# Optimization experiments

Hardware: AMD Instinct MI355X
Metric: run time of the kernel (lower is better)

Reference implementation:

```python
import jax, jax.numpy as jnp
import numpy as np

EPS_SINKHORN = 0.01   # entropic regularization (cost / eps)
EPS_LOG = 1e-8        # numerical epsilon inside logs
NUM_ITERS = 50


def setup_inputs() -> dict:
    key = jax.random.key(0)
    k1, k2 = jax.random.split(key)
    B, N = 8, 2048
    x1 = jax.random.normal(k1, (B, N, 3), dtype=jnp.float32)
    x2 = jax.random.normal(k2, (B, N, 3), dtype=jnp.float32)
    return {"x1": x1, "x2": x2}


def reference(x1, x2):
    # x1, x2: [B, N, 3] point clouds
    B, N, _ = x1.shape
    # pairwise squared-distance cost matrix: [B, N, N]
    cost = jnp.sum((x1[:, :, None, :] - x2[:, None, :, :]) ** 2, axis=-1)
    K = jnp.exp(-cost / EPS_SINKHORN)  # constant across iterations

    inv_n = jnp.float32(1.0 / N)
    mu = jnp.full((B, N), inv_n, dtype=cost.dtype)
    nu = jnp.full((B, N), inv_n, dtype=cost.dtype)
    log_mu = jnp.log(mu + EPS_LOG)
    log_nu = jnp.log(nu + EPS_LOG)

    def step(carry, _):
        u, v = carry
        # row update: sum_j K_ij * exp(v_j)
        u = log_mu - jnp.log(jnp.einsum('bij,bj->bi', K, jnp.exp(v)) + EPS_LOG)
        # col update: sum_i K_ij * exp(u_i)
        v = log_nu - jnp.log(jnp.einsum('bij,bi->bj', K, jnp.exp(u)) + EPS_LOG)
        return (u, v), None

    u0 = jnp.zeros((B, N), dtype=cost.dtype)
    v0 = jnp.zeros((B, N), dtype=cost.dtype)
    (u, v), _ = jax.lax.scan(step, (u0, v0), None, length=NUM_ITERS)

    transport = K * jnp.exp(u[:, :, None] + v[:, None, :])  # [B, N, N]
    emd = jnp.sum(transport * cost, axis=(1, 2))            # [B]
    return emd
```

## Files before the change

kernel.cpp:

```cpp
#include <hip/hip_runtime.h>
#include <cmath>

#define BATCH 8
#define NPT   2048
#define NPAIR (NPT / 2)
#define NPTS  (BATCH * NPT)
#define TILES 64
#define GRID_MAIN 256
#define THREADS 1024
#define ITERS 50

#define C_LOG2E 1.4426950408889634f
#define NEG100C (-144.26950408889634f)
#define S200C   288.53900817779268f
#define EPS_LOG 1e-8f
#define LN2_01  0.006931471805599453f

typedef float v2f __attribute__((ext_vector_type(2)));
typedef float v4f __attribute__((ext_vector_type(4)));
typedef unsigned long long u64t;

static __device__ __forceinline__ float fast_exp2(float x) {
#if __has_builtin(__builtin_amdgcn_exp2f)
    return __builtin_amdgcn_exp2f(x);
#else
    return exp2f(x);
#endif
}

static __device__ __forceinline__ v2f pk_fma(v2f a, v2f b, v2f c) {
    v2f d;
    asm("v_pk_fma_f32 %0, %1, %2, %3" : "=v"(d) : "v"(a), "v"(b), "v"(c));
    return d;
}
static __device__ __forceinline__ v2f pk_add(v2f a, v2f b) {
    v2f d;
    asm("v_pk_add_f32 %0, %1, %2" : "=v"(d) : "v"(a), "v"(b));
    return d;
}

static __device__ __forceinline__ float gload(const float* p) {
    return __hip_atomic_load(p, __ATOMIC_RELAXED, __HIP_MEMORY_SCOPE_AGENT);
}
static __device__ __forceinline__ void gstore(float* p, float val) {
    __hip_atomic_store(p, val, __ATOMIC_RELAXED, __HIP_MEMORY_SCOPE_AGENT);
}
static __device__ __forceinline__ u64t gload2(const float* p) {
    return __hip_atomic_load((const u64t*)p, __ATOMIC_RELAXED,
                             __HIP_MEMORY_SCOPE_AGENT);
}

__global__ void init_kernel(float* __restrict__ out,
                            unsigned int* __restrict__ flags) {
    int t = threadIdx.x;
    if (t < BATCH) out[t] = 0.0f;
    flags[t] = 0u;
}

static __device__ __forceinline__ void bar_arrive(unsigned int* flags,
                                                  int slot, unsigned int ph) {
    __syncthreads();
    if (threadIdx.x == 0)
        __hip_atomic_store(&flags[slot], ph, __ATOMIC_RELAXED,
                           __HIP_MEMORY_SCOPE_AGENT);
}
static __device__ __forceinline__ void bar_wait(const unsigned int* bflags,
                                                int wave, int lane,
                                                unsigned int ph) {
    if (wave == 0) {
        while (__hip_atomic_load(&bflags[lane], __ATOMIC_RELAXED,
                                 __HIP_MEMORY_SCOPE_AGENT) < ph) {
            __builtin_amdgcn_s_sleep(1);
        }
    }
    __syncthreads();
    __builtin_amdgcn_sched_barrier(0);
}

static __device__ __forceinline__ float half_core(
        const v4f* cdXY, const v4f* cdZW, int p0,
        v2f RX, v2f RY, v2f RZ, v2f RC)
{
    float accx = 0.0f, accy = 0.0f;
#pragma unroll 4
    for (int s = 0; s < 32; s++) {
        v4f a  = cdXY[p0 + s];
        v4f bz = cdZW[p0 + s];
        v2f xx = __builtin_shufflevector(a,  a,  0, 1);
        v2f yy = __builtin_shufflevector(a,  a,  2, 3);
        v2f zz = __builtin_shufflevector(bz, bz, 0, 1);
        v2f ww = __builtin_shufflevector(bz, bz, 2, 3);
        v2f t = pk_fma(xx, RX, ww);
        t = pk_fma(yy, RY, t);
        t = pk_fma(zz, RZ, t);
        t = pk_add(t, RC);
        accx += fast_exp2(t.x);
        accy += fast_exp2(t.y);
    }
    return accx + accy;
}

__global__ __launch_bounds__(THREADS, 4) void sinkhorn_kernel(
        const float* __restrict__ x1, const float* __restrict__ x2,
        float* __restrict__ u, float* __restrict__ v,
        unsigned int* __restrict__ flags, float* __restrict__ out)
{
    __shared__ v4f c1XY[2][NPAIR], c1ZW[2][NPAIR];
    __shared__ v4f c2XY[2][NPAIR], c2ZW[2][NPAIR];
    __shared__ float part[32][17];

    const int b0   = blockIdx.x / TILES;
    const int tile = blockIdx.x % TILES;
    const int bA = b0, bB = b0 + 4;
    const int baseA = bA * NPT, baseB = bB * NPT;
    const int slotA = bA * TILES + tile, slotB = bB * TILES + tile;
    const unsigned int* flA = flags + bA * TILES;
    const unsigned int* flB = flags + bB * TILES;

    const int tid  = threadIdx.x;
    const int wave = tid >> 6;
    const int lane = tid & 63;
    const int rloc = lane & 31;
    const int ch   = lane >> 5;
    const int row  = tile * 32 + rloc;
    const int p0   = wave * 64 + ch * 32;

    const float log_mu = logf(1.0f / (float)NPT + EPS_LOG);

    float P1a[2], P1b[2], P2a[2], P2b[2];
#pragma unroll
    for (int g = 0; g < 2; g++) {
        int base = g ? baseB : baseA;
        const float* p = x1 + 3 * (base + 2 * tid);
        float ax = p[0], ay = p[1], az = p[2];
        float bx = p[3], by = p[4], bz = p[5];
        float na = fmaf(ax, ax, fmaf(ay, ay, az * az));
        float nb = fmaf(bx, bx, fmaf(by, by, bz * bz));
        P1a[g] = na * NEG100C;  P1b[g] = nb * NEG100C;
        c1XY[g][tid] = (v4f){ax * S200C, bx * S200C, ay * S200C, by * S200C};
        c1ZW[g][tid] = (v4f){az * S200C, bz * S200C, P1a[g], P1b[g]};

        p = x2 + 3 * (base + 2 * tid);
        ax = p[0]; ay = p[1]; az = p[2];
        bx = p[3]; by = p[4]; bz = p[5];
        na = fmaf(ax, ax, fmaf(ay, ay, az * az));
        nb = fmaf(bx, bx, fmaf(by, by, bz * bz));
        P2a[g] = na * NEG100C;  P2b[g] = nb * NEG100C;
        c2XY[g][tid] = (v4f){ax * S200C, bx * S200C, ay * S200C, by * S200C};
        c2ZW[g][tid] = (v4f){az * S200C, bz * S200C, P2a[g], P2b[g]};
    }

    v2f RX1[2], RY1[2], RZ1[2], RC1[2], RX2[2], RY2[2], RZ2[2], RC2[2];
    float rc1s[2];
#pragma unroll
    for (int g = 0; g < 2; g++) {
        int base = g ? baseB : baseA;
        const float* p = x1 + 3 * (base + row);
        float a = p[0], bb = p[1], c = p[2];
        float nn = NEG100C * fmaf(a, a, fmaf(bb, bb, c * c));
        RX1[g] = (v2f){a, a};  RY1[g] = (v2f){bb, bb};
        RZ1[g] = (v2f){c, c};  RC1[g] = (v2f){nn, nn};
        rc1s[g] = nn;
        p = x2 + 3 * (base + row);
        a = p[0]; bb = p[1]; c = p[2];
        nn = NEG100C * fmaf(a, a, fmaf(bb, bb, c * c));
        RX2[g] = (v2f){a, a};  RY2[g] = (v2f){bb, bb};
        RZ2[g] = (v2f){c, c};  RC2[g] = (v2f){nn, nn};
    }
    __syncthreads();

    auto reduce_store = [&](float s, float* dst) {
        s += __shfl_xor(s, 32, 64);
        if (lane < 32) part[rloc][wave] = s;
        __syncthreads();
        if (wave == 0) {
            float t = 0.0f;
#pragma unroll
            for (int w = 0; w < 16; w++) t += part[rloc][w];
            float res = log_mu - __logf(t + EPS_LOG);
            if (lane < 32) gstore(dst, res);
        }
    };
    auto fold_u = [&](int g) {
        u64t d = gload2(u + (g ? baseB : baseA) + 2 * tid);
        reinterpret_cast<v2f*>(&c1ZW[g][tid])[1] = (v2f){
            fmaf(C_LOG2E, __uint_as_float((unsigned)d), P1a[g]),
            fmaf(C_LOG2E, __uint_as_float((unsigned)(d >> 32)), P1b[g])};
        __syncthreads();
    };
    auto fold_v = [&](int g) {
        u64t d = gload2(v + (g ? baseB : baseA) + 2 * tid);
        reinterpret_cast<v2f*>(&c2ZW[g][tid])[1] = (v2f){
            fmaf(C_LOG2E, __uint_as_float((unsigned)d), P2a[g]),
            fmaf(C_LOG2E, __uint_as_float((unsigned)(d >> 32)), P2b[g])};
        __syncthreads();
    };
    auto comp_u = [&](int g) {
        float s = half_core(c2XY[g], c2ZW[g], p0,
                            RX1[g], RY1[g], RZ1[g], RC1[g]);
        reduce_store(s, u + (g ? baseB : baseA) + row);
    };
    auto comp_v = [&](int g) {
        float s = half_core(c1XY[g], c1ZW[g], p0,
                            RX2[g], RY2[g], RZ2[g], RC2[g]);
        reduce_store(s, v + (g ? baseB : baseA) + row);
    };

    comp_u(0); bar_arrive(flags, slotA, 1);
    comp_u(1); bar_arrive(flags, slotB, 1);

    for (int it = 0; it < ITERS; it++) {
        const unsigned pu = 2 * it + 1, pv = 2 * it + 2;
        bar_wait(flA, wave, lane, pu);
        fold_u(0);
        comp_v(0); bar_arrive(flags, slotA, pv);
        bar_wait(flB, wave, lane, pu);
        fold_u(1);
        comp_v(1); bar_arrive(flags, slotB, pv);
        bar_wait(flA, wave, lane, pv);
        fold_v(0);
        if (it < ITERS - 1) { comp_u(0); bar_arrive(flags, slotA, pu + 2); }
        bar_wait(flB, wave, lane, pv);
        fold_v(1);
        if (it < ITERS - 1) { comp_u(1); bar_arrive(flags, slotB, pu + 2); }
    }

    v2f* cvp0 = reinterpret_cast<v2f*>(c1XY[0]);
    v2f* cvp1 = reinterpret_cast<v2f*>(c1XY[1]);
    {
        u64t dA = gload2(v + baseA + 2 * tid);
        u64t dB = gload2(v + baseB + 2 * tid);
        cvp0[tid] = (v2f){0.01f * __uint_as_float((unsigned)dA),
                          0.01f * __uint_as_float((unsigned)(dA >> 32))};
        cvp1[tid] = (v2f){0.01f * __uint_as_float((unsigned)dB),
                          0.01f * __uint_as_float((unsigned)(dB >> 32))};
    }
    __syncthreads();

    const v2f NL2 = {-LN2_01, -LN2_01};
    float es[2];
#pragma unroll
    for (int g = 0; g < 2; g++) {
        int base = g ? baseB : baseA;
        v2f* cvp = g ? cvp1 : cvp0;
        float ur = gload(&u[base + row]);
        float rcs = fmaf(C_LOG2E, ur, rc1s[g]);
        v2f RCC = (v2f){rcs, rcs};
        float sus = 0.01f * ur;
        v2f SU = (v2f){sus, sus};
        v2f eacc = {0.0f, 0.0f};
#pragma unroll 4
        for (int s = 0; s < 32; s++) {
            v4f a   = c2XY[g][p0 + s];
            v4f bz  = c2ZW[g][p0 + s];
            v2f cv2 = cvp[p0 + s];
            v2f xx = __builtin_shufflevector(a,  a,  0, 1);
            v2f yy = __builtin_shufflevector(a,  a,  2, 3);
            v2f zz = __builtin_shufflevector(bz, bz, 0, 1);
            v2f ww = __builtin_shufflevector(bz, bz, 2, 3);
            v2f t = pk_fma(xx, RX1[g], ww);
            t = pk_fma(yy, RY1[g], t);
            t = pk_fma(zz, RZ1[g], t);
            t = pk_add(t, RCC);
            v2f c2 = pk_fma(t, NL2, pk_add(SU, cv2));
            eacc.x = fmaf(fast_exp2(t.x), c2.x, eacc.x);
            eacc.y = fmaf(fast_exp2(t.y), c2.y, eacc.y);
        }
        float e = eacc.x + eacc.y;
#pragma unroll
        for (int m = 32; m >= 1; m >>= 1) e += __shfl_xor(e, m, 64);
        es[g] = e;
    }

    if (lane == 0) { part[0][wave] = es[0]; part[1][wave] = es[1]; }
    __syncthreads();
    if (tid == 0) {
        float sA = 0.0f, sB = 0.0f;
#pragma unroll
        for (int w = 0; w < 16; w++) { sA += part[0][w]; sB += part[1][w]; }
        atomicAdd(&out[bA], sA);
        atomicAdd(&out[bB], sB);
    }
}

extern "C" void kernel_launch(void* const* d_in, const int* in_sizes, int n_in,
                              void* d_out, int out_size, void* d_ws, size_t ws_size,
                              hipStream_t stream) {
    (void)in_sizes; (void)n_in; (void)out_size; (void)ws_size;
    const float* x1 = (const float*)d_in[0];
    const float* x2 = (const float*)d_in[1];
    float* out = (float*)d_out;

    char* ws = (char*)d_ws;
    float* u = (float*)ws;
    float* v = u + NPTS;
    unsigned int* flags = (unsigned int*)(v + NPTS);

    init_kernel<<<1, 512, 0, stream>>>(out, flags);
    sinkhorn_kernel<<<GRID_MAIN, THREADS, 0, stream>>>(x1, x2, u, v, flags, out);
}
```

Measured before the change: 825.3 us.

## Register-block two rows per thread and drop per-fold block barriers

Each thread now handles two rows (16 lanes per row group instead of 32), so every shared-memory load of column data feeds two rows' distance and exp computations, halving LDS traffic per exp. The __syncthreads after fold_u/fold_v is removed and the final reduction reads partial sums as vec4 from a padded 16-byte-aligned buffer. The packed inline asm is replaced by plain vector arithmetic the compiler can schedule. Removing the fold barriers relies on the reduce barrier and bar_wait's __syncthreads for ordering, and the extra per-row registers raise register pressure.

```diff
diff --git a/kernel.cpp b/kernel.cpp
--- a/kernel.cpp
+++ b/kernel.cpp
@@ -28,17 +28,6 @@
 #endif
 }
 
-static __device__ __forceinline__ v2f pk_fma(v2f a, v2f b, v2f c) {
-    v2f d;
-    asm("v_pk_fma_f32 %0, %1, %2, %3" : "=v"(d) : "v"(a), "v"(b), "v"(c));
-    return d;
-}
-static __device__ __forceinline__ v2f pk_add(v2f a, v2f b) {
-    v2f d;
-    asm("v_pk_add_f32 %0, %1, %2" : "=v"(d) : "v"(a), "v"(b));
-    return d;
-}
-
 static __device__ __forceinline__ float gload(const float* p) {
     return __hip_atomic_load(p, __ATOMIC_RELAXED, __HIP_MEMORY_SCOPE_AGENT);
 }
@@ -64,11 +53,11 @@
         __hip_atomic_store(&flags[slot], ph, __ATOMIC_RELAXED,
                            __HIP_MEMORY_SCOPE_AGENT);
 }
-static __device__ __forceinline__ void bar_wait(const unsigned int* bflags,
+static __device__ __forceinline__ void bar_wait(const unsigned int* bf,
                                                 int wave, int lane,
                                                 unsigned int ph) {
     if (wave == 0) {
-        while (__hip_atomic_load(&bflags[lane], __ATOMIC_RELAXED,
+        while (__hip_atomic_load(&bf[lane], __ATOMIC_RELAXED,
                                  __HIP_MEMORY_SCOPE_AGENT) < ph) {
             __builtin_amdgcn_s_sleep(1);
         }
@@ -77,27 +66,34 @@
     __builtin_amdgcn_sched_barrier(0);
 }
 
-static __device__ __forceinline__ float half_core(
+static __device__ __forceinline__ v2f half_core2(
         const v4f* cdXY, const v4f* cdZW, int p0,
-        v2f RX, v2f RY, v2f RZ, v2f RC)
+        const v2f (&RX)[2], const v2f (&RY)[2],
+        const v2f (&RZ)[2], const v2f (&RC)[2])
 {
-    float accx = 0.0f, accy = 0.0f;
+    v2f a0 = {0.0f, 0.0f}, a1 = {0.0f, 0.0f};
 #pragma unroll 4
-    for (int s = 0; s < 32; s++) {
-        v4f a  = cdXY[p0 + s];
-        v4f bz = cdZW[p0 + s];
-        v2f xx = __builtin_shufflevector(a,  a,  0, 1);
-        v2f yy = __builtin_shufflevector(a,  a,  2, 3);
-        v2f zz = __builtin_shufflevector(bz, bz, 0, 1);
-        v2f ww = __builtin_shufflevector(bz, bz, 2, 3);
-        v2f t = pk_fma(xx, RX, ww);
-        t = pk_fma(yy, RY, t);
-        t = pk_fma(zz, RZ, t);
-        t = pk_add(t, RC);
-        accx += fast_exp2(t.x);
-        accy += fast_exp2(t.y);
-    }
-    return accx + accy;
+    for (int s = 0; s < 16; s++) {
+        v4f A = cdXY[p0 + 4 * s];
+        v4f B = cdZW[p0 + 4 * s];
+        v2f xx = __builtin_shufflevector(A, A, 0, 1);
+        v2f yy = __builtin_shufflevector(A, A, 2, 3);
+        v2f zz = __builtin_shufflevector(B, B, 0, 1);
+        v2f ww = __builtin_shufflevector(B, B, 2, 3);
+        v2f t0 = xx * RX[0] + ww;
+        t0 = yy * RY[0] + t0;
+        t0 = zz * RZ[0] + t0;
+        t0 = t0 + RC[0];
+        v2f t1 = xx * RX[1] + ww;
+        t1 = yy * RY[1] + t1;
+        t1 = zz * RZ[1] + t1;
+        t1 = t1 + RC[1];
+        a0.x += fast_exp2(t0.x);
+        a0.y += fast_exp2(t0.y);
+        a1.x += fast_exp2(t1.x);
+        a1.y += fast_exp2(t1.y);
+    }
+    return (v2f){a0.x + a0.y, a1.x + a1.y};
 }
 
 __global__ __launch_bounds__(THREADS, 4) void sinkhorn_kernel(
@@ -107,7 +103,7 @@
 {
     __shared__ v4f c1XY[2][NPAIR], c1ZW[2][NPAIR];
     __shared__ v4f c2XY[2][NPAIR], c2ZW[2][NPAIR];
-    __shared__ float part[32][17];
+    __shared__ __align__(16) float part[32][20];
 
     const int b0   = blockIdx.x / TILES;
     const int tile = blockIdx.x % TILES;
@@ -120,10 +116,9 @@
     const int tid  = threadIdx.x;
     const int wave = tid >> 6;
     const int lane = tid & 63;
-    const int rloc = lane & 31;
-    const int ch   = lane >> 5;
-    const int row  = tile * 32 + rloc;
-    const int p0   = wave * 64 + ch * 32;
+    const int rloc = lane & 15;
+    const int ch   = lane >> 4;
+    const int p0   = wave * 64 + ch;
 
     const float log_mu = logf(1.0f / (float)NPT + EPS_LOG);
 
@@ -150,35 +145,52 @@
         c2ZW[g][tid] = (v4f){az * S200C, bz * S200C, P2a[g], P2b[g]};
     }
 
-    v2f RX1[2], RY1[2], RZ1[2], RC1[2], RX2[2], RY2[2], RZ2[2], RC2[2];
-    float rc1s[2];
+    v2f RX1[2][2], RY1[2][2], RZ1[2][2], RC1[2][2];
+    v2f RX2[2][2], RY2[2][2], RZ2[2][2], RC2[2][2];
+    float rc1s[2][2];
 #pragma unroll
     for (int g = 0; g < 2; g++) {
         int base = g ? baseB : baseA;
-        const float* p = x1 + 3 * (base + row);
-        float a = p[0], bb = p[1], c = p[2];
-        float nn = NEG100C * fmaf(a, a, fmaf(bb, bb, c * c));
-        RX1[g] = (v2f){a, a};  RY1[g] = (v2f){bb, bb};
-        RZ1[g] = (v2f){c, c};  RC1[g] = (v2f){nn, nn};
-        rc1s[g] = nn;
-        p = x2 + 3 * (base + row);
-        a = p[0]; bb = p[1]; c = p[2];
-        nn = NEG100C * fmaf(a, a, fmaf(bb, bb, c * c));
-        RX2[g] = (v2f){a, a};  RY2[g] = (v2f){bb, bb};
-        RZ2[g] = (v2f){c, c};  RC2[g] = (v2f){nn, nn};
-    }
-    __syncthreads();
-
-    auto reduce_store = [&](float s, float* dst) {
-        s += __shfl_xor(s, 32, 64);
-        if (lane < 32) part[rloc][wave] = s;
+#pragma unroll
+        for (int rr = 0; rr < 2; rr++) {
+            int row = tile * 32 + rloc + 16 * rr;
+            const float* p = x1 + 3 * (base + row);
+            float a = p[0], bb = p[1], c = p[2];
+            float nn = NEG100C * fmaf(a, a, fmaf(bb, bb, c * c));
+            RX1[g][rr] = (v2f){a, a};  RY1[g][rr] = (v2f){bb, bb};
+            RZ1[g][rr] = (v2f){c, c};  RC1[g][rr] = (v2f){nn, nn};
+            rc1s[g][rr] = nn;
+            p = x2 + 3 * (base + row);
+            a = p[0]; bb = p[1]; c = p[2];
+            nn = NEG100C * fmaf(a, a, fmaf(bb, bb, c * c));
+            RX2[g][rr] = (v2f){a, a};  RY2[g][rr] = (v2f){bb, bb};
+            RZ2[g][rr] = (v2f){c, c};  RC2[g][rr] = (v2f){nn, nn};
+        }
+    }
+    __syncthreads();
+
+    auto do_phase = [&](const v4f* XY, const v4f* ZW,
+                        const v2f (&RX)[2], const v2f (&RY)[2],
+                        const v2f (&RZ)[2], const v2f (&RC)[2],
+                        float* drow) {
+        v2f s2 = half_core2(XY, ZW, p0, RX, RY, RZ, RC);
+        s2.x += __shfl_xor(s2.x, 16, 64);
+        s2.x += __shfl_xor(s2.x, 32, 64);
+        s2.y += __shfl_xor(s2.y, 16, 64);
+        s2.y += __shfl_xor(s2.y, 32, 64);
+        if (lane < 16) {
+            part[rloc][wave]      = s2.x;
+            part[rloc + 16][wave] = s2.y;
+        }
         __syncthreads();
-        if (wave == 0) {
-            float t = 0.0f;
-#pragma unroll
-            for (int w = 0; w < 16; w++) t += part[rloc][w];
-            float res = log_mu - __logf(t + EPS_LOG);
-            if (lane < 32) gstore(dst, res);
+        if (wave == 0 && lane < 32) {
+            const v4f* pr = reinterpret_cast<const v4f*>(&part[lane][0]);
+            v4f q0 = pr[0], q1 = pr[1], q2 = pr[2], q3 = pr[3];
+            float t = ((q0.x + q0.y) + (q0.z + q0.w)) +
+                      ((q1.x + q1.y) + (q1.z + q1.w)) +
+                      ((q2.x + q2.y) + (q2.z + q2.w)) +
+                      ((q3.x + q3.y) + (q3.z + q3.w));
+            gstore(drow + lane, log_mu - __logf(t + EPS_LOG));
         }
     };
     auto fold_u = [&](int g) {
@@ -186,54 +198,61 @@
         reinterpret_cast<v2f*>(&c1ZW[g][tid])[1] = (v2f){
             fmaf(C_LOG2E, __uint_as_float((unsigned)d), P1a[g]),
             fmaf(C_LOG2E, __uint_as_float((unsigned)(d >> 32)), P1b[g])};
-        __syncthreads();
     };
     auto fold_v = [&](int g) {
         u64t d = gload2(v + (g ? baseB : baseA) + 2 * tid);
         reinterpret_cast<v2f*>(&c2ZW[g][tid])[1] = (v2f){
             fmaf(C_LOG2E, __uint_as_float((unsigned)d), P2a[g]),
             fmaf(C_LOG2E, __uint_as_float((unsigned)(d >> 32)), P2b[g])};
-        __syncthreads();
     };
-    auto comp_u = [&](int g) {
-        float s = half_core(c2XY[g], c2ZW[g], p0,
-                            RX1[g], RY1[g], RZ1[g], RC1[g]);
-        reduce_store(s, u + (g ? baseB : baseA) + row);
-    };
-    auto comp_v = [&](int g) {
-        float s = half_core(c1XY[g], c1ZW[g], p0,
-                            RX2[g], RY2[g], RZ2[g], RC2[g]);
-        reduce_store(s, v + (g ? baseB : baseA) + row);
-    };
-
-    comp_u(0); bar_arrive(flags, slotA, 1);
-    comp_u(1); bar_arrive(flags, slotB, 1);
+
+    float* uA = u + baseA + tile * 32;  float* uB = u + baseB + tile * 32;
+    float* vA = v + baseA + tile * 32;  float* vB = v + baseB + tile * 32;
+
+    do_phase(c2XY[0], c2ZW[0], RX1[0], RY1[0], RZ1[0], RC1[0], uA);
+    bar_arrive(flags, slotA, 1);
+    do_phase(c2XY[1], c2ZW[1], RX1[1], RY1[1], RZ1[1], RC1[1], uB);
+    bar_arrive(flags, slotB, 1);
 
     for (int it = 0; it < ITERS; it++) {
         const unsigned pu = 2 * it + 1, pv = 2 * it + 2;
         bar_wait(flA, wave, lane, pu);
         fold_u(0);
-        comp_v(0); bar_arrive(flags, slotA, pv);
+        do_phase(c1XY[0], c1ZW[0], RX2[0], RY2[0], RZ2[0], RC2[0], vA);
+        bar_arrive(flags, slotA, pv);
         bar_wait(flB, wave, lane, pu);
         fold_u(1);
-        comp_v(1); bar_arrive(flags, slotB, pv);
-        bar_wait(flA, wave, lane, pv);
-        fold_v(0);
-        if (it < ITERS - 1) { comp_u(0); bar_arrive(flags, slotA, pu + 2); }
-        bar_wait(flB, wave, lane, pv);
-        fold_v(1);
-        if (it < ITERS - 1) { comp_u(1); bar_arrive(flags, slotB, pu + 2); }
-    }
+        do_phase(c1XY[1], c1ZW[1], RX2[1], RY2[1], RZ2[1], RC2[1], vB);
+        bar_arrive(flags, slotB, pv);
+        if (it < ITERS - 1) {
+            bar_wait(flA, wave, lane, pv);
+            fold_v(0);
+            do_phase(c2XY[0], c2ZW[0], RX1[0], RY1[0], RZ1[0], RC1[0], uA);
+            bar_arrive(flags, slotA, pu + 2);
+            bar_wait(flB, wave, lane, pv);
+            fold_v(1);
+            do_phase(c2XY[1], c2ZW[1], RX1[1], RY1[1], RZ1[1], RC1[1], uB);
+            bar_arrive(flags, slotB, pu + 2);
+        }
+    }
+    bar_wait(flA, wave, lane, 2 * ITERS);
+    bar_wait(flB, wave, lane, 2 * ITERS);
 
     v2f* cvp0 = reinterpret_cast<v2f*>(c1XY[0]);
     v2f* cvp1 = reinterpret_cast<v2f*>(c1XY[1]);
     {
         u64t dA = gload2(v + baseA + 2 * tid);
         u64t dB = gload2(v + baseB + 2 * tid);
-        cvp0[tid] = (v2f){0.01f * __uint_as_float((unsigned)dA),
-                          0.01f * __uint_as_float((unsigned)(dA >> 32))};
-        cvp1[tid] = (v2f){0.01f * __uint_as_float((unsigned)dB),
-                          0.01f * __uint_as_float((unsigned)(dB >> 32))};
+        float aA = __uint_as_float((unsigned)dA);
+        float bA2 = __uint_as_float((unsigned)(dA >> 32));
+        float aB = __uint_as_float((unsigned)dB);
+        float bB2 = __uint_as_float((unsigned)(dB >> 32));
+        reinterpret_cast<v2f*>(&c2ZW[0][tid])[1] =
+            (v2f){fmaf(C_LOG2E, aA, P2a[0]), fmaf(C_LOG2E, bA2, P2b[0])};
+        reinterpret_cast<v2f*>(&c2ZW[1][tid])[1] =
+            (v2f){fmaf(C_LOG2E, aB, P2a[1]), fmaf(C_LOG2E, bB2, P2b[1])};
+        cvp0[tid] = (v2f){0.01f * aA, 0.01f * bA2};
+        cvp1[tid] = (v2f){0.01f * aB, 0.01f * bB2};
     }
     __syncthreads();
 
@@ -243,30 +262,39 @@
     for (int g = 0; g < 2; g++) {
         int base = g ? baseB : baseA;
         v2f* cvp = g ? cvp1 : cvp0;
-        float ur = gload(&u[base + row]);
-        float rcs = fmaf(C_LOG2E, ur, rc1s[g]);
-        v2f RCC = (v2f){rcs, rcs};
-        float sus = 0.01f * ur;
-        v2f SU = (v2f){sus, sus};
-        v2f eacc = {0.0f, 0.0f};
+        float ur0 = gload(&u[base + tile * 32 + rloc]);
+        float ur1 = gload(&u[base + tile * 32 + rloc + 16]);
+        float r0 = fmaf(C_LOG2E, ur0, rc1s[g][0]);
+        float r1 = fmaf(C_LOG2E, ur1, rc1s[g][1]);
+        v2f RCC0 = (v2f){r0, r0}, RCC1 = (v2f){r1, r1};
+        v2f SU0 = (v2f){0.01f * ur0, 0.01f * ur0};
+        v2f SU1 = (v2f){0.01f * ur1, 0.01f * ur1};
+        v2f e0 = {0.0f, 0.0f}, e1 = {0.0f, 0.0f};
 #pragma unroll 4
-        for (int s = 0; s < 32; s++) {
-            v4f a   = c2XY[g][p0 + s];
-            v4f bz  = c2ZW[g][p0 + s];
-            v2f cv2 = cvp[p0 + s];
-            v2f xx = __builtin_shufflevector(a,  a,  0, 1);
-            v2f yy = __builtin_shufflevector(a,  a,  2, 3);
-            v2f zz = __builtin_shufflevector(bz, bz, 0, 1);
-            v2f ww = __builtin_shufflevector(bz, bz, 2, 3);
-            v2f t = pk_fma(xx, RX1[g], ww);
-            t = pk_fma(yy, RY1[g], t);
-            t = pk_fma(zz, RZ1[g], t);
-            t = pk_add(t, RCC);
-            v2f c2 = pk_fma(t, NL2, pk_add(SU, cv2));
-            eacc.x = fmaf(fast_exp2(t.x), c2.x, eacc.x);
-            eacc.y = fmaf(fast_exp2(t.y), c2.y, eacc.y);
-        }
-        float e = eacc.x + eacc.y;
+        for (int s = 0; s < 16; s++) {
+            v4f A   = c2XY[g][p0 + 4 * s];
+            v4f B   = c2ZW[g][p0 + 4 * s];
+            v2f cv2 = cvp[p0 + 4 * s];
+            v2f xx = __builtin_shufflevector(A, A, 0, 1);
+            v2f yy = __builtin_shufflevector(A, A, 2, 3);
+            v2f zz = __builtin_shufflevector(B, B, 0, 1);
+            v2f ww = __builtin_shufflevector(B, B, 2, 3);
+            v2f t0 = xx * RX1[g][0] + ww;
+            t0 = yy * RY1[g][0] + t0;
+            t0 = zz * RZ1[g][0] + t0;
+            t0 = t0 + RCC0;
+            v2f c20 = t0 * NL2 + (SU0 + cv2);
+            e0.x = fmaf(fast_exp2(t0.x), c20.x, e0.x);
+            e0.y = fmaf(fast_exp2(t0.y), c20.y, e0.y);
+            v2f t1 = xx * RX1[g][1] + ww;
+            t1 = yy * RY1[g][1] + t1;
+            t1 = zz * RZ1[g][1] + t1;
+            t1 = t1 + RCC1;
+            v2f c21 = t1 * NL2 + (SU1 + cv2);
+            e1.x = fmaf(fast_exp2(t1.x), c21.x, e1.x);
+            e1.y = fmaf(fast_exp2(t1.y), c21.y, e1.y);
+        }
+        float e = (e0.x + e0.y) + (e1.x + e1.y);
 #pragma unroll
         for (int m = 32; m >= 1; m >>= 1) e += __shfl_xor(e, m, 64);
         es[g] = e;
```

Result: faster. 785.2 us (-4.9%).
